# Performance work log

Measured on AMD Instinct MI355X. Metric: run time of the kernel, lower is better.

Reference implementation:

```python
import jax, jax.numpy as jnp
import numpy as np

B, T, H, C = 32, 2048, 1024, 1024

def setup_inputs() -> dict:
    key = jax.random.key(0)
    k1, k2, k3, k4, k5, k6 = jax.random.split(key, 6)
    decoder_output = jax.random.normal(k1, (B, 1, H), dtype=jnp.float32)
    encoder_outputs = jax.random.normal(k2, (B, T, H), dtype=jnp.float32)
    scale = 1.0 / np.sqrt(H)
    W = jax.random.normal(k3, (H, C), dtype=jnp.float32) * scale
    V = jax.random.normal(k4, (H, C), dtype=jnp.float32) * scale
    b = jax.random.uniform(k5, (C,), dtype=jnp.float32, minval=-0.1, maxval=0.1)
    w = jax.random.normal(k6, (C, 1), dtype=jnp.float32) * (1.0 / np.sqrt(C))
    return {"decoder_output": decoder_output, "encoder_outputs": encoder_outputs,
            "W": W, "V": V, "b": b, "w": w}

def reference(decoder_output, encoder_outputs, W, V, b, w):
    # Additive (Bahdanau) content attention.
    dec_proj = jnp.einsum('bqh,hc->bqc', decoder_output, W)   # [B,1,C]
    enc_proj = jnp.einsum('bth,hc->btc', encoder_outputs, V)  # [B,T,C]
    energy = jnp.tanh(dec_proj + enc_proj + b)                # [B,T,C]
    scores = jnp.einsum('btc,c->bt', energy, w[:, 0])         # [B,T]
    alignment = jax.nn.softmax(scores, axis=-1)               # [B,T]
    context = jnp.einsum('bt,bth->bh', alignment, encoder_outputs)  # [B,H]
    return context
```

## Files before the change

### kernel.cpp

```cpp
#include <hip/hip_runtime.h>
#include <hip/hip_bf16.h>
#include <stdint.h>

#define Bn 32
#define Tn 2048
#define Hn 1024
#define Cn 1024

typedef short short8 __attribute__((ext_vector_type(8)));
typedef float floatx4 __attribute__((ext_vector_type(4)));

__device__ __forceinline__ unsigned int bf16_rne(float f) {
    union { float f; unsigned int u; } v; v.f = f;
    unsigned int u = v.u;
    return (u + 0x7fffu + ((u >> 16) & 1u)) >> 16;
}

__global__ void k_prep(const float* __restrict__ dec, const float* __restrict__ W,
                       const float* __restrict__ bias, const float* __restrict__ V,
                       float* __restrict__ dbp, uint4* __restrict__ vp) {
    if (blockIdx.x < 512) {
        const int blk = blockIdx.x;
        const int b  = blk >> 4;
        const int y  = (blk >> 2) & 3;
        const int z  = blk & 3;
        const int c  = y * 256 + threadIdx.x;
        const int h0 = z * 256;
        const float* dv = dec + b * Hn + h0;
        const float* wp = W + (size_t)h0 * Cn + c;
        float acc = 0.f;
#pragma unroll 8
        for (int h = 0; h < 256; ++h)
            acc += dv[h] * wp[(size_t)h * Cn];
        if (z == 0) acc += bias[c];
        dbp[(size_t)(b * 4 + z) * Cn + c] = acc;
    } else {
        const int vb   = blockIdx.x - 512;
        const int sub  = threadIdx.x >> 6;
        const int lane = threadIdx.x & 63;
        const int bid  = vb * 4 + sub;
        const int nt   = bid >> 5;
        const int kt   = bid & 31;
        const int c    = nt * 16 + (lane & 15);
        const int k0   = kt * 32 + (lane >> 4) * 8;
        unsigned int h[8];
#pragma unroll
        for (int j = 0; j < 8; ++j)
            h[j] = bf16_rne(V[(size_t)(k0 + j) * Cn + c]);
        uint4 u;
        u.x = h[0] | (h[1] << 16);
        u.y = h[2] | (h[3] << 16);
        u.z = h[4] | (h[5] << 16);
        u.w = h[6] | (h[7] << 16);
        vp[(size_t)bid * 64 + lane] = u;
    }
}

#define BLK_M 64
#define LDA   1032

struct ScoresShared {
    unsigned short A[BLK_M * LDA];
    float scores[BLK_M];
};

__global__ __launch_bounds__(512, 2)
void k_scores(const float* __restrict__ enc, const uint4* __restrict__ vp,
              const float* __restrict__ dbp, const float* __restrict__ wv,
              float* __restrict__ scores_g) {
    __shared__ ScoresShared sh;
    const int tid  = threadIdx.x;
    const int lane = tid & 63;
    const int wave = tid >> 6;
    const int lhi  = lane >> 4;
    const int llo  = lane & 15;

    float4 fbuf[32];
    {
        const float4* ep = (const float4*)(enc + (size_t)(blockIdx.x * 4) * BLK_M * Hn);
#pragma unroll
        for (int i = 0; i < 32; ++i)
            fbuf[i] = ep[tid + i * 512];
    }

    for (int q = 0; q < 4; ++q) {
        const int tile = blockIdx.x * 4 + q;
        const int b    = tile >> 5;
        const int row0 = tile * BLK_M;

        if (tid < BLK_M) sh.scores[tid] = 0.f;

#pragma unroll
        for (int i = 0; i < 32; ++i) {
            int idx = tid + i * 512;
            int r   = idx >> 8;
            int c4  = idx & 255;
            uint2 p;
            p.x = bf16_rne(fbuf[i].x) | (bf16_rne(fbuf[i].y) << 16);
            p.y = bf16_rne(fbuf[i].z) | (bf16_rne(fbuf[i].w) << 16);
            *(uint2*)&sh.A[r * LDA + c4 * 4] = p;
        }
        __syncthreads();

        if (q < 3) {
            const float4* ep = (const float4*)(enc + (size_t)(tile + 1) * BLK_M * Hn);
#pragma unroll
            for (int i = 0; i < 32; ++i)
                fbuf[i] = ep[tid + i * 512];
        }

        float score_part[16];
#pragma unroll
        for (int i = 0; i < 16; ++i) score_part[i] = 0.f;

        for (int ni = 0; ni < 2; ++ni) {
            const int colbase = (ni * 8 + wave) * 64;
            const int nt0     = colbase >> 4;

            floatx4 acc[4][4];
#pragma unroll
            for (int i = 0; i < 4; ++i)
#pragma unroll
                for (int j = 0; j < 4; ++j)
                    acc[i][j] = (floatx4){0.f, 0.f, 0.f, 0.f};

#pragma unroll 2
            for (int kt = 0; kt < 32; ++kt) {
                short8 afr[4], bfr[4];
#pragma unroll
                for (int rg = 0; rg < 4; ++rg) {
                    const unsigned short* ap = &sh.A[(rg * 16 + llo) * LDA + kt * 32 + lhi * 8];
                    afr[rg] = *(const short8*)ap;
                }
#pragma unroll
                for (int j = 0; j < 4; ++j) {
                    uint4 u = vp[((nt0 + j) * 32 + kt) * 64 + lane];
                    bfr[j] = __builtin_bit_cast(short8, u);
                }
#pragma unroll
                for (int rg = 0; rg < 4; ++rg)
#pragma unroll
                    for (int j = 0; j < 4; ++j)
                        acc[rg][j] = __builtin_amdgcn_mfma_f32_16x16x32_bf16(
                            afr[rg], bfr[j], acc[rg][j], 0, 0, 0);
            }

#pragma unroll
            for (int j = 0; j < 4; ++j) {
                const int c  = colbase + j * 16 + llo;
                const float db = dbp[(size_t)(b * 4 + 0) * Cn + c]
                               + dbp[(size_t)(b * 4 + 1) * Cn + c]
                               + dbp[(size_t)(b * 4 + 2) * Cn + c]
                               + dbp[(size_t)(b * 4 + 3) * Cn + c];
                const float wc = wv[c];
#pragma unroll
                for (int rg = 0; rg < 4; ++rg) {
#pragma unroll
                    for (int r = 0; r < 4; ++r) {
                        float x = acc[rg][j][r] + db;
                        x = fminf(fmaxf(x, -12.f), 12.f);
                        float e = __expf(2.f * x);
                        float t = 1.f - 2.f / (e + 1.f);
                        score_part[rg * 4 + r] += t * wc;
                    }
                }
            }
        }

#pragma unroll
        for (int i = 0; i < 16; ++i) {
            float v = score_part[i];
            v += __shfl_xor(v, 1);
            v += __shfl_xor(v, 2);
            v += __shfl_xor(v, 4);
            v += __shfl_xor(v, 8);
            score_part[i] = v;
        }
        if (llo == 0) {
#pragma unroll
            for (int rg = 0; rg < 4; ++rg)
#pragma unroll
                for (int r = 0; r < 4; ++r)
                    atomicAdd(&sh.scores[rg * 16 + lhi * 4 + r], score_part[rg * 4 + r]);
        }
        __syncthreads();
        if (tid < BLK_M) scores_g[row0 + tid] = sh.scores[tid];
    }
}

__global__ void k_ctx1(const float* __restrict__ enc, const float* __restrict__ scores,
                       float* __restrict__ part) {
    const int b   = blockIdx.x;
    const int tc  = blockIdx.y;
    const int tid = threadIdx.x;
    __shared__ float al_sh[256];
    __shared__ float red[4];
    __shared__ float red2[4];

    const float* s = scores + b * Tn;
    float v[8];
    float lmax = -1e30f;
#pragma unroll
    for (int i = 0; i < 8; ++i) { v[i] = s[tid + i * 256]; lmax = fmaxf(lmax, v[i]); }
    for (int off = 1; off < 64; off <<= 1) lmax = fmaxf(lmax, __shfl_xor(lmax, off));
    if ((tid & 63) == 0) red[tid >> 6] = lmax;
    __syncthreads();
    lmax = fmaxf(fmaxf(red[0], red[1]), fmaxf(red[2], red[3]));
    float lsum = 0.f;
#pragma unroll
    for (int i = 0; i < 8; ++i) lsum += __expf(v[i] - lmax);
    for (int off = 1; off < 64; off <<= 1) lsum += __shfl_xor(lsum, off);
    if ((tid & 63) == 0) red2[tid >> 6] = lsum;
    __syncthreads();
    lsum = red2[0] + red2[1] + red2[2] + red2[3];
    const float inv = 1.f / lsum;
    al_sh[tid] = __expf(s[tc * 256 + tid] - lmax) * inv;
    __syncthreads();

    const float4* ep = (const float4*)(enc + ((size_t)b * Tn + tc * 256) * Hn);
    float4 acc = {0.f, 0.f, 0.f, 0.f};
#pragma unroll 4
    for (int t = 0; t < 256; ++t) {
        const float a = al_sh[t];
        const float4 e = ep[t * 256 + tid];
        acc.x += a * e.x; acc.y += a * e.y; acc.z += a * e.z; acc.w += a * e.w;
    }
    ((float4*)part)[(b * 8 + tc) * 256 + tid] = acc;
}

__global__ void k_ctx2(const float* __restrict__ part, float* __restrict__ out) {
    const int b   = blockIdx.x;
    const int tid = threadIdx.x;
    const float4* pp = (const float4*)part;
    float4 s = {0.f, 0.f, 0.f, 0.f};
#pragma unroll
    for (int tc = 0; tc < 8; ++tc) {
        float4 p = pp[(b * 8 + tc) * 256 + tid];
        s.x += p.x; s.y += p.y; s.z += p.z; s.w += p.w;
    }
    ((float4*)out)[b * 256 + tid] = s;
}

extern "C" void kernel_launch(void* const* d_in, const int* in_sizes, int n_in,
                              void* d_out, int out_size, void* d_ws, size_t ws_size,
                              hipStream_t stream) {
    const float* dec  = (const float*)d_in[0];
    const float* enc  = (const float*)d_in[1];
    const float* W    = (const float*)d_in[2];
    const float* V    = (const float*)d_in[3];
    const float* bias = (const float*)d_in[4];
    const float* wv   = (const float*)d_in[5];
    float* out = (float*)d_out;

    char* ws = (char*)d_ws;
    float* dbp    = (float*)(ws);
    uint4* vpack  = (uint4*)(ws + 524288);
    float* scores = (float*)(ws + 524288 + 2097152);
    float* cpart  = (float*)(ws + 524288 + 2097152 + 262144);

    k_prep  <<<1024, 256, 0, stream>>>(dec, W, bias, V, dbp, vpack);
    k_scores<<<256, 512, 0, stream>>>(enc, vpack, dbp, wv, scores);
    k_ctx1  <<<dim3(32, 8), 256, 0, stream>>>(enc, scores, cpart);
    k_ctx2  <<<32, 256, 0, stream>>>(cpart, out);
}
```

Baseline: 649.3 us.

## Use one tile per scores block and split context reduction into finer chunks

The scores kernel drops its four-tile persistent loop with register prefetch of the next tile and instead launches 1024 blocks that each load, convert and process a single 64-row tile. The context kernel splits T into 32 chunks of 64 rows instead of 8 chunks of 256, giving 1024 blocks and more partial sums for the final reduction. The aim is better GPU occupancy and load balance across CUs. The cost is losing the software overlap of the next tile's global load with MFMA work, plus more partial-sum traffic.

```diff
diff --git a/kernel.cpp b/kernel.cpp
--- a/kernel.cpp
+++ b/kernel.cpp
@@ -69,123 +69,109 @@
               const float* __restrict__ dbp, const float* __restrict__ wv,
               float* __restrict__ scores_g) {
     __shared__ ScoresShared sh;
+    const int wg   = blockIdx.x;
     const int tid  = threadIdx.x;
     const int lane = tid & 63;
     const int wave = tid >> 6;
+    const int b    = wg >> 5;
+    const int row0 = wg * BLK_M;
     const int lhi  = lane >> 4;
     const int llo  = lane & 15;
 
-    float4 fbuf[32];
+    if (tid < BLK_M) sh.scores[tid] = 0.f;
+
     {
-        const float4* ep = (const float4*)(enc + (size_t)(blockIdx.x * 4) * BLK_M * Hn);
-#pragma unroll
-        for (int i = 0; i < 32; ++i)
-            fbuf[i] = ep[tid + i * 512];
-    }
-
-    for (int q = 0; q < 4; ++q) {
-        const int tile = blockIdx.x * 4 + q;
-        const int b    = tile >> 5;
-        const int row0 = tile * BLK_M;
-
-        if (tid < BLK_M) sh.scores[tid] = 0.f;
-
-#pragma unroll
-        for (int i = 0; i < 32; ++i) {
-            int idx = tid + i * 512;
+        const float4* ep = (const float4*)(enc + (size_t)row0 * Hn);
+#pragma unroll 4
+        for (int it = 0; it < 32; ++it) {
+            int idx = tid + it * 512;
             int r   = idx >> 8;
             int c4  = idx & 255;
+            float4 f = ep[r * 256 + c4];
             uint2 p;
-            p.x = bf16_rne(fbuf[i].x) | (bf16_rne(fbuf[i].y) << 16);
-            p.y = bf16_rne(fbuf[i].z) | (bf16_rne(fbuf[i].w) << 16);
+            p.x = bf16_rne(f.x) | (bf16_rne(f.y) << 16);
+            p.y = bf16_rne(f.z) | (bf16_rne(f.w) << 16);
             *(uint2*)&sh.A[r * LDA + c4 * 4] = p;
         }
-        __syncthreads();
-
-        if (q < 3) {
-            const float4* ep = (const float4*)(enc + (size_t)(tile + 1) * BLK_M * Hn);
-#pragma unroll
-            for (int i = 0; i < 32; ++i)
-                fbuf[i] = ep[tid + i * 512];
+    }
+    __syncthreads();
+
+    float score_part[16];
+#pragma unroll
+    for (int i = 0; i < 16; ++i) score_part[i] = 0.f;
+
+    for (int ni = 0; ni < 2; ++ni) {
+        const int colbase = (ni * 8 + wave) * 64;
+        const int nt0     = colbase >> 4;
+
+        floatx4 acc[4][4];
+#pragma unroll
+        for (int i = 0; i < 4; ++i)
+#pragma unroll
+            for (int j = 0; j < 4; ++j)
+                acc[i][j] = (floatx4){0.f, 0.f, 0.f, 0.f};
+
+#pragma unroll 2
+        for (int kt = 0; kt < 32; ++kt) {
+            short8 afr[4], bfr[4];
+#pragma unroll
+            for (int rg = 0; rg < 4; ++rg) {
+                const unsigned short* ap = &sh.A[(rg * 16 + llo) * LDA + kt * 32 + lhi * 8];
+                afr[rg] = *(const short8*)ap;
+            }
+#pragma unroll
+            for (int j = 0; j < 4; ++j) {
+                uint4 u = vp[((nt0 + j) * 32 + kt) * 64 + lane];
+                bfr[j] = __builtin_bit_cast(short8, u);
+            }
+#pragma unroll
+            for (int rg = 0; rg < 4; ++rg)
+#pragma unroll
+                for (int j = 0; j < 4; ++j)
+                    acc[rg][j] = __builtin_amdgcn_mfma_f32_16x16x32_bf16(
+                        afr[rg], bfr[j], acc[rg][j], 0, 0, 0);
         }
 
-        float score_part[16];
-#pragma unroll
-        for (int i = 0; i < 16; ++i) score_part[i] = 0.f;
-
-        for (int ni = 0; ni < 2; ++ni) {
-            const int colbase = (ni * 8 + wave) * 64;
-            const int nt0     = colbase >> 4;
-
-            floatx4 acc[4][4];
-#pragma unroll
-            for (int i = 0; i < 4; ++i)
-#pragma unroll
-                for (int j = 0; j < 4; ++j)
-                    acc[i][j] = (floatx4){0.f, 0.f, 0.f, 0.f};
-
-#pragma unroll 2
-            for (int kt = 0; kt < 32; ++kt) {
-                short8 afr[4], bfr[4];
-#pragma unroll
-                for (int rg = 0; rg < 4; ++rg) {
-                    const unsigned short* ap = &sh.A[(rg * 16 + llo) * LDA + kt * 32 + lhi * 8];
-                    afr[rg] = *(const short8*)ap;
-                }
-#pragma unroll
-                for (int j = 0; j < 4; ++j) {
-                    uint4 u = vp[((nt0 + j) * 32 + kt) * 64 + lane];
-                    bfr[j] = __builtin_bit_cast(short8, u);
-                }
-#pragma unroll
-                for (int rg = 0; rg < 4; ++rg)
-#pragma unroll
-                    for (int j = 0; j < 4; ++j)
-                        acc[rg][j] = __builtin_amdgcn_mfma_f32_16x16x32_bf16(
-                            afr[rg], bfr[j], acc[rg][j], 0, 0, 0);
-            }
-
-#pragma unroll
-            for (int j = 0; j < 4; ++j) {
-                const int c  = colbase + j * 16 + llo;
-                const float db = dbp[(size_t)(b * 4 + 0) * Cn + c]
-                               + dbp[(size_t)(b * 4 + 1) * Cn + c]
-                               + dbp[(size_t)(b * 4 + 2) * Cn + c]
-                               + dbp[(size_t)(b * 4 + 3) * Cn + c];
-                const float wc = wv[c];
-#pragma unroll
-                for (int rg = 0; rg < 4; ++rg) {
-#pragma unroll
-                    for (int r = 0; r < 4; ++r) {
-                        float x = acc[rg][j][r] + db;
-                        x = fminf(fmaxf(x, -12.f), 12.f);
-                        float e = __expf(2.f * x);
-                        float t = 1.f - 2.f / (e + 1.f);
-                        score_part[rg * 4 + r] += t * wc;
-                    }
+#pragma unroll
+        for (int j = 0; j < 4; ++j) {
+            const int c  = colbase + j * 16 + llo;
+            const float db = dbp[(size_t)(b * 4 + 0) * Cn + c]
+                           + dbp[(size_t)(b * 4 + 1) * Cn + c]
+                           + dbp[(size_t)(b * 4 + 2) * Cn + c]
+                           + dbp[(size_t)(b * 4 + 3) * Cn + c];
+            const float wc = wv[c];
+#pragma unroll
+            for (int rg = 0; rg < 4; ++rg) {
+#pragma unroll
+                for (int r = 0; r < 4; ++r) {
+                    float x = acc[rg][j][r] + db;
+                    x = fminf(fmaxf(x, -12.f), 12.f);
+                    float e = __expf(2.f * x);
+                    float t = 1.f - 2.f / (e + 1.f);
+                    score_part[rg * 4 + r] += t * wc;
                 }
             }
         }
-
-#pragma unroll
-        for (int i = 0; i < 16; ++i) {
-            float v = score_part[i];
-            v += __shfl_xor(v, 1);
-            v += __shfl_xor(v, 2);
-            v += __shfl_xor(v, 4);
-            v += __shfl_xor(v, 8);
-            score_part[i] = v;
-        }
-        if (llo == 0) {
-#pragma unroll
-            for (int rg = 0; rg < 4; ++rg)
-#pragma unroll
-                for (int r = 0; r < 4; ++r)
-                    atomicAdd(&sh.scores[rg * 16 + lhi * 4 + r], score_part[rg * 4 + r]);
-        }
-        __syncthreads();
-        if (tid < BLK_M) scores_g[row0 + tid] = sh.scores[tid];
-    }
+    }
+
+#pragma unroll
+    for (int i = 0; i < 16; ++i) {
+        float v = score_part[i];
+        v += __shfl_xor(v, 1);
+        v += __shfl_xor(v, 2);
+        v += __shfl_xor(v, 4);
+        v += __shfl_xor(v, 8);
+        score_part[i] = v;
+    }
+    if (llo == 0) {
+#pragma unroll
+        for (int rg = 0; rg < 4; ++rg)
+#pragma unroll
+            for (int r = 0; r < 4; ++r)
+                atomicAdd(&sh.scores[rg * 16 + lhi * 4 + r], score_part[rg * 4 + r]);
+    }
+    __syncthreads();
+    if (tid < BLK_M) scores_g[row0 + tid] = sh.scores[tid];
 }
 
 __global__ void k_ctx1(const float* __restrict__ enc, const float* __restrict__ scores,
@@ -193,7 +179,7 @@
     const int b   = blockIdx.x;
     const int tc  = blockIdx.y;
     const int tid = threadIdx.x;
-    __shared__ float al_sh[256];
+    __shared__ float al_sh[64];
     __shared__ float red[4];
     __shared__ float red2[4];
 
@@ -214,18 +200,18 @@
     __syncthreads();
     lsum = red2[0] + red2[1] + red2[2] + red2[3];
     const float inv = 1.f / lsum;
-    al_sh[tid] = __expf(s[tc * 256 + tid] - lmax) * inv;
-    __syncthreads();
-
-    const float4* ep = (const float4*)(enc + ((size_t)b * Tn + tc * 256) * Hn);
+    if (tid < 64) al_sh[tid] = __expf(s[tc * 64 + tid] - lmax) * inv;
+    __syncthreads();
+
+    const float4* ep = (const float4*)(enc + ((size_t)b * Tn + tc * 64) * Hn);
     float4 acc = {0.f, 0.f, 0.f, 0.f};
-#pragma unroll 4
-    for (int t = 0; t < 256; ++t) {
+#pragma unroll 8
+    for (int t = 0; t < 64; ++t) {
         const float a = al_sh[t];
         const float4 e = ep[t * 256 + tid];
         acc.x += a * e.x; acc.y += a * e.y; acc.z += a * e.z; acc.w += a * e.w;
     }
-    ((float4*)part)[(b * 8 + tc) * 256 + tid] = acc;
+    ((float4*)part)[(b * 32 + tc) * 256 + tid] = acc;
 }
 
 __global__ void k_ctx2(const float* __restrict__ part, float* __restrict__ out) {
@@ -234,8 +220,8 @@
     const float4* pp = (const float4*)part;
     float4 s = {0.f, 0.f, 0.f, 0.f};
 #pragma unroll
-    for (int tc = 0; tc < 8; ++tc) {
-        float4 p = pp[(b * 8 + tc) * 256 + tid];
+    for (int tc = 0; tc < 32; ++tc) {
+        float4 p = pp[(b * 32 + tc) * 256 + tid];
         s.x += p.x; s.y += p.y; s.z += p.z; s.w += p.w;
     }
     ((float4*)out)[b * 256 + tid] = s;
@@ -259,7 +245,7 @@
     float* cpart  = (float*)(ws + 524288 + 2097152 + 262144);
 
     k_prep  <<<1024, 256, 0, stream>>>(dec, W, bias, V, dbp, vpack);
-    k_scores<<<256, 512, 0, stream>>>(enc, vpack, dbp, wv, scores);
-    k_ctx1  <<<dim3(32, 8), 256, 0, stream>>>(enc, scores, cpart);
+    k_scores<<<1024, 512, 0, stream>>>(enc, vpack, dbp, wv, scores);
+    k_ctx1  <<<dim3(32, 32), 256, 0, stream>>>(enc, scores, cpart);
     k_ctx2  <<<32, 256, 0, stream>>>(cpart, out);
 }
```

After: 562.7 us. -13.3%, faster.
